# Performance work log

Measured on AMD Instinct MI355X. Metric: run time of the kernel, lower is better.

## Reference

```python
import jax, jax.numpy as jnp
import numpy as np

H, DH, PE = 8, 64, 32
SCALE = DH ** -0.5


def setup_inputs() -> dict:
    key = jax.random.key(0)
    ks = jax.random.split(key, 12)
    B, L, D, K, G = 2, 4096, 256, 16, 4
    inner = H * DH
    kv_in = D + PE
    return {
        "spatial": jax.random.normal(ks[0], (B, L, D), jnp.float32),
        "topk_indices": jax.random.randint(ks[1], (B, L, K), 0, L, jnp.int32),
        "rpe": jax.random.normal(ks[2], (B, L, K, PE), jnp.float32),
        "self_rpe": jax.random.normal(ks[3], (B, L, 1, PE), jnp.float32),
        "distances": jax.random.uniform(ks[4], (B, L, K), jnp.float32) * 10.0,
        "global_latents": jax.random.normal(ks[5], (B, G, D), jnp.float32),
        "Wq": jax.random.normal(ks[6], (D, inner), jnp.float32) * (D ** -0.5),
        "Wk": jax.random.normal(ks[7], (kv_in, inner), jnp.float32) * (kv_in ** -0.5),
        "Wv": jax.random.normal(ks[8], (kv_in, inner), jnp.float32) * (kv_in ** -0.5),
        "Wo": jax.random.normal(ks[9], (inner, D), jnp.float32) * (inner ** -0.5),
        "bo": jnp.zeros((D,), jnp.float32),
        "log_sigma": jnp.full((H,), np.log(3.0), jnp.float32),
        "global_bias": jnp.zeros((), jnp.float32),
    }


def reference(spatial, topk_indices, rpe, self_rpe, distances, global_latents,
              Wq, Wk, Wv, Wo, bo, log_sigma, global_bias):
    B, L, D = spatial.shape
    k = topk_indices.shape[-1]
    G = global_latents.shape[1]
    dt = spatial.dtype

    # gather per-query neighbor features: [B, L, k, D]
    neighbors = jax.vmap(lambda s, idx: s[idx])(spatial, topk_indices)

    # context = [self, neighbors, globals] -> [B, L, c, D], c = 1 + k + G
    ctx = jnp.concatenate([
        spatial[:, :, None, :],
        neighbors,
        jnp.broadcast_to(global_latents[:, None, :, :], (B, L, G, D)),
    ], axis=2)

    # RPE concat on feature dim (self_rpe, rpe, zeros for globals)
    rpe_cat = jnp.concatenate([
        self_rpe, rpe, jnp.zeros((B, L, G, PE), dt)
    ], axis=2)
    ctx = jnp.concatenate([ctx, rpe_cat], axis=-1)  # [B, L, c, D+PE]

    Q = (spatial @ Wq).reshape(B, L, H, DH).transpose(0, 2, 1, 3)          # bhld
    Kt = (ctx @ Wk).reshape(B, L, 1 + k + G, H, DH).transpose(0, 3, 1, 2, 4)  # bhlcd
    Vt = (ctx @ Wv).reshape(B, L, 1 + k + G, H, DH).transpose(0, 3, 1, 2, 4)

    attn = jnp.einsum('bhld,bhlcd->bhlc', Q, Kt) * SCALE

    # gaussian distance bias on local (self + k neighbors) slots
    sigma_sq = jnp.exp(log_sigma) ** 2                     # [H]
    dist_local = jnp.concatenate([jnp.zeros((B, L, 1), dt), distances], axis=2)  # [B,L,1+k]
    gauss = -(dist_local ** 2)[:, None, :, :] / (2.0 * sigma_sq[None, :, None, None])
    bias = jnp.concatenate([
        gauss,
        jnp.broadcast_to(global_bias, (B, H, L, G)).astype(dt),
    ], axis=-1)
    attn = attn + bias

    w = jax.nn.softmax(attn, axis=-1)
    out = jnp.einsum('bhlc,bhlcd->bhld', w, Vt)
    out = out.transpose(0, 2, 1, 3).reshape(B, L, H * DH)
    return out @ Wo + bo
```

## Files before the change

### kernel.cpp

```cpp
#include <hip/hip_runtime.h>
#include <hip/hip_bf16.h>

#define BB 2
#define LL 4096
#define DD 256
#define KK 16
#define GG 4
#define HH 8
#define DH 64
#define PE 32
#define INNER 512
#define CC 21
#define MM (BB*LL)
#define SCALE 0.125f
#define NT1 1792
#define KT1 256
#define NT2 256
#define KT2 768

typedef unsigned short u16;
typedef __attribute__((ext_vector_type(8))) short bf16x8;
typedef __attribute__((ext_vector_type(4))) float f32x4;
typedef unsigned short ushort4_t __attribute__((ext_vector_type(4)));
typedef unsigned short ushort8_t __attribute__((ext_vector_type(8)));

static __device__ __forceinline__ float bf2f(unsigned short u) {
    return __uint_as_float(((unsigned)u) << 16);
}
static __device__ __forceinline__ unsigned short f2bf(float f) {
    unsigned u = __float_as_uint(f);
    unsigned r = u + 0x7fffu + ((u >> 16) & 1u);
    return (unsigned short)(r >> 16);
}
static __device__ __forceinline__ void gld_lds16(const void* g, void* l) {
    __builtin_amdgcn_global_load_lds(
        (const __attribute__((address_space(1))) unsigned int*)g,
        (__attribute__((address_space(3))) unsigned int*)l, 16, 0, 0);
}

__global__ __launch_bounds__(256) void prep_A(
    const float* __restrict__ Wq, const float* __restrict__ Wk,
    float* __restrict__ A)
{
    const int e = blockIdx.x;
    const int tid = threadIdx.x;
    __shared__ float qrow[INNER];
    qrow[tid]       = Wq[e * INNER + tid];
    qrow[tid + 256] = Wq[e * INNER + 256 + tid];
    __syncthreads();
    const int h = tid >> 5, p = tid & 31;
    const float* __restrict__ wr = &Wk[(size_t)(DD + p) * INNER + h * DH];
    const float* __restrict__ qh = &qrow[h * DH];
    float s = 0.f;
    #pragma unroll 8
    for (int d = 0; d < DH; ++d) s += wr[d] * qh[d];
    A[e * 256 + tid] = s;
}

__global__ __launch_bounds__(256) void prep_M2(
    const float* __restrict__ Wv, const float* __restrict__ Wo,
    float* __restrict__ M2)
{
    const int hp = blockIdx.x;
    const int h = hp >> 5, p = hp & 31;
    const int tid = threadIdx.x;
    __shared__ float vrow[DH];
    if (tid < DH) vrow[tid] = Wv[(size_t)(DD + p) * INNER + h * DH + tid];
    __syncthreads();
    float s = 0.f;
    #pragma unroll 8
    for (int d = 0; d < DH; ++d) s += vrow[d] * Wo[(size_t)(h * DH + d) * DD + tid];
    M2[hp * 256 + tid] = s;
}

__global__ __launch_bounds__(256) void cast_spatial(
    const float* __restrict__ in, u16* __restrict__ out)
{
    const size_t i = ((size_t)blockIdx.x * 256 + threadIdx.x) * 8;
    float4 a = *reinterpret_cast<const float4*>(&in[i]);
    float4 b = *reinterpret_cast<const float4*>(&in[i + 4]);
    ushort8_t v = { f2bf(a.x), f2bf(a.y), f2bf(a.z), f2bf(a.w),
                    f2bf(b.x), f2bf(b.y), f2bf(b.z), f2bf(b.w) };
    *reinterpret_cast<ushort8_t*>(&out[i]) = v;
}

__global__ __launch_bounds__(256) void prep_wcat_t(
    const float* __restrict__ Wq, const float* __restrict__ Wk,
    const float* __restrict__ Wv, const float* __restrict__ A,
    u16* __restrict__ Wt)
{
    const int n0 = blockIdx.x * 64;
    const int k0 = blockIdx.y * 64;
    const float* src; int ld, nloc;
    if (n0 < 512)       { src = Wq; ld = INNER; nloc = n0; }
    else if (n0 < 1024) { src = Wk; ld = INNER; nloc = n0 - 512; }
    else if (n0 < 1536) { src = Wv; ld = INNER; nloc = n0 - 1024; }
    else                { src = A;  ld = 256;   nloc = n0 - 1536; }

    __shared__ float tile[64][65];
    const int tid = threadIdx.x;
    const int tk = tid >> 4;
    const int tn = (tid & 15) * 4;
    #pragma unroll
    for (int rep = 0; rep < 4; ++rep) {
        const int k = k0 + tk + rep * 16;
        float4 v = *reinterpret_cast<const float4*>(&src[(size_t)k * ld + nloc + tn]);
        tile[tk + rep * 16][tn + 0] = v.x; tile[tk + rep * 16][tn + 1] = v.y;
        tile[tk + rep * 16][tn + 2] = v.z; tile[tk + rep * 16][tn + 3] = v.w;
    }
    __syncthreads();
    const int wn = tid >> 2;
    const int wk = (tid & 3) * 16;
    ushort8_t o0, o1;
    #pragma unroll
    for (int i = 0; i < 8; ++i) o0[i] = f2bf(tile[wk + i][wn]);
    #pragma unroll
    for (int i = 0; i < 8; ++i) o1[i] = f2bf(tile[wk + 8 + i][wn]);
    u16* dst = &Wt[(size_t)(n0 + wn) * KT1 + k0 + wk];
    *reinterpret_cast<ushort8_t*>(dst)     = o0;
    *reinterpret_cast<ushort8_t*>(dst + 8) = o1;
}

__global__ __launch_bounds__(256) void prep_wout_t(
    const float* __restrict__ Wo, const float* __restrict__ M2,
    u16* __restrict__ Wot)
{
    const int n0 = blockIdx.x * 64;
    const int k0 = blockIdx.y * 64;
    const float* src; int krow;
    if (k0 < 512) { src = Wo; krow = k0; }
    else          { src = M2; krow = k0 - 512; }

    __shared__ float tile[64][65];
    const int tid = threadIdx.x;
    const int tk = tid >> 4;
    const int tn = (tid & 15) * 4;
    #pragma unroll
    for (int rep = 0; rep < 4; ++rep) {
        const int k = krow + tk + rep * 16;
        float4 v = *reinterpret_cast<const float4*>(&src[(size_t)k * DD + n0 + tn]);
        tile[tk + rep * 16][tn + 0] = v.x; tile[tk + rep * 16][tn + 1] = v.y;
        tile[tk + rep * 16][tn + 2] = v.z; tile[tk + rep * 16][tn + 3] = v.w;
    }
    __syncthreads();
    const int wn = tid >> 2;
    const int wk = (tid & 3) * 16;
    ushort8_t o0, o1;
    #pragma unroll
    for (int i = 0; i < 8; ++i) o0[i] = f2bf(tile[wk + i][wn]);
    #pragma unroll
    for (int i = 0; i < 8; ++i) o1[i] = f2bf(tile[wk + 8 + i][wn]);
    u16* dst = &Wot[(size_t)(n0 + wn) * KT2 + k0 + wk];
    *reinterpret_cast<ushort8_t*>(dst)     = o0;
    *reinterpret_cast<ushort8_t*>(dst + 8) = o1;
}

template<int KT, int LDA, int NTOT, int BN, bool F32OUT>
__global__ __launch_bounds__(256) void mfma_gemm(
    const u16* __restrict__ A, const u16* __restrict__ Bt,
    u16* __restrict__ outB, float* __restrict__ outF,
    const float* __restrict__ bias)
{
    constexpr int WNT = BN / 2;
    constexpr int BJ  = WNT / 16;
    constexpr int BCH = BN / 8;

    __shared__ u16 As[128 * 64];
    __shared__ u16 Bs[BN * 64];

    const int tid  = threadIdx.x;
    const int lane = tid & 63;
    const int w    = tid >> 6;
    const int wr   = w >> 1, wc = w & 1;
    const int m0 = blockIdx.x * 128;
    const int n0 = blockIdx.y * BN;
    const int fr = lane & 15, fq = lane >> 4;

    f32x4 acc[4][BJ];
    #pragma unroll
    for (int i = 0; i < 4; ++i)
        #pragma unroll
        for (int j = 0; j < BJ; ++j)
            acc[i][j] = (f32x4){0.f, 0.f, 0.f, 0.f};

    for (int t = 0; t < KT / 64; ++t) {
        const int k0 = t * 64;
        #pragma unroll
        for (int cc = 0; cc < 4; ++cc) {
            const int chunk = w + cc * 4;
            gld_lds16(A + (size_t)(m0 + chunk * 8 + (lane >> 3)) * LDA + k0 + (lane & 7) * 8,
                      (char*)&As[0] + chunk * 1024);
        }
        #pragma unroll
        for (int cc = 0; cc < BCH / 4; ++cc) {
            const int chunk = w + cc * 4;
            gld_lds16(Bt + (size_t)(n0 + chunk * 8 + (lane >> 3)) * KT + k0 + (lane & 7) * 8,
                      (char*)&Bs[0] + chunk * 1024);
        }
        __syncthreads();
        #pragma unroll
        for (int ks = 0; ks < 2; ++ks) {
            bf16x8 av[4], bv[BJ];
            #pragma unroll
            for (int i = 0; i < 4; ++i)
                av[i] = *reinterpret_cast<const bf16x8*>(
                    &As[(wr * 64 + i * 16 + fr) * 64 + ks * 32 + fq * 8]);
            #pragma unroll
            for (int j = 0; j < BJ; ++j)
                bv[j] = *reinterpret_cast<const bf16x8*>(
                    &Bs[(wc * WNT + j * 16 + fr) * 64 + ks * 32 + fq * 8]);
            #pragma unroll
            for (int i = 0; i < 4; ++i)
                #pragma unroll
                for (int j = 0; j < BJ; ++j)
                    acc[i][j] = __builtin_amdgcn_mfma_f32_16x16x32_bf16(
                        av[i], bv[j], acc[i][j], 0, 0, 0);
        }
        __syncthreads();
    }

    #pragma unroll
    for (int i = 0; i < 4; ++i)
        #pragma unroll
        for (int j = 0; j < BJ; ++j)
            #pragma unroll
            for (int rgi = 0; rgi < 4; ++rgi) {
                const int row = m0 + wr * 64 + i * 16 + fq * 4 + rgi;
                const int col = n0 + wc * WNT + j * 16 + fr;
                if constexpr (F32OUT)
                    outF[(size_t)row * NTOT + col] = acc[i][j][rgi] + bias[col];
                else
                    outB[(size_t)row * NTOT + col] = f2bf(acc[i][j][rgi]);
            }
}

__global__ __launch_bounds__(256) void gemm_globals(
    const float* __restrict__ gl, const float* __restrict__ Wk,
    const float* __restrict__ Wv, u16* __restrict__ Kg, u16* __restrict__ Vg)
{
    const int bg  = blockIdx.x;
    const int tid = threadIdx.x;
    const int col = blockIdx.y * 128 + (tid & 127);
    const bool isv = tid >= 128;
    const float* __restrict__ W = isv ? Wv : Wk;
    const float* __restrict__ x = &gl[bg * DD];
    float s = 0.f;
    #pragma unroll 4
    for (int k = 0; k < DD; ++k) s += x[k] * W[(size_t)k * INNER + col];
    if (isv) Vg[bg * INNER + col] = f2bf(s);
    else     Kg[bg * INNER + col] = f2bf(s);
}

__global__ __launch_bounds__(256) void attn_kernel(
    const u16* __restrict__ X, const u16* __restrict__ Kg,
    const u16* __restrict__ Vg, const int* __restrict__ topk,
    const float* __restrict__ rpe, const float* __restrict__ self_rpe,
    const float* __restrict__ distances, const float* __restrict__ log_sigma,
    const float* __restrict__ global_bias, u16* __restrict__ ob2)
{
    const int lane = threadIdx.x & 63;
    const int q = __builtin_amdgcn_readfirstlane(blockIdx.x * 4 + (threadIdx.x >> 6));
    const int b = q >> 12;
    const int h = lane >> 3;
    const int r = lane & 7;
    const int qk = q * KK;
    const size_t bL = (size_t)b * LL;
    const int bG = b * GG;

    float qf[8];
    {
        ushort8_t qv = *reinterpret_cast<const ushort8_t*>(&X[(size_t)q * NT1 + lane * 8]);
        #pragma unroll
        for (int j = 0; j < 8; ++j) qf[j] = bf2f(qv[j]);
    }
    float t4[4];
    {
        ushort4_t tu = *reinterpret_cast<const ushort4_t*>(
            &X[(size_t)q * NT1 + 1536 + h * 32 + r * 4]);
        t4[0] = bf2f(tu[0]); t4[1] = bf2f(tu[1]);
        t4[2] = bf2f(tu[2]); t4[3] = bf2f(tu[3]);
    }

    const float inv2sig = 0.5f * __expf(-2.f * log_sigma[h]);
    const float gbias   = global_bias[0];

    float m = -1e30f, denom = 0.f;
    float acc[8] = {0.f,0.f,0.f,0.f,0.f,0.f,0.f,0.f};
    float rb[4]  = {0.f,0.f,0.f,0.f};

    #pragma unroll
    for (int c = 0; c < CC; ++c) {
        const u16 *kb, *vb;
        const float* rp_ = nullptr;
        float biasc;
        if (c == 0) {
            kb = &X[(size_t)q * NT1 + 512]; vb = &X[(size_t)q * NT1 + 1024];
            rp_ = &self_rpe[(size_t)q * PE];
            biasc = 0.f;
        } else if (c < 17) {
            const int idx = topk[qk + c - 1];
            const u16* row = &X[(bL + idx) * NT1];
            kb = row + 512; vb = row + 1024;
            rp_ = &rpe[((size_t)qk + (c - 1)) * PE];
            const float d = distances[qk + c - 1];
            biasc = -(d * d) * inv2sig;
        } else {
            kb = &Kg[(size_t)(bG + c - 17) * INNER];
            vb = &Vg[(size_t)(bG + c - 17) * INNER];
            biasc = gbias;
        }
        ushort8_t kv = *reinterpret_cast<const ushort8_t*>(kb + lane * 8);
        ushort8_t vv = *reinterpret_cast<const ushort8_t*>(vb + lane * 8);
        float4 r4 = {0.f,0.f,0.f,0.f};
        if (c < 17) r4 = *reinterpret_cast<const float4*>(rp_ + r * 4);

        float part = bf2f(kv[0])*qf[0] + bf2f(kv[1])*qf[1]
                   + bf2f(kv[2])*qf[2] + bf2f(kv[3])*qf[3]
                   + bf2f(kv[4])*qf[4] + bf2f(kv[5])*qf[5]
                   + bf2f(kv[6])*qf[6] + bf2f(kv[7])*qf[7];
        if (c < 17)
            part += r4.x*t4[0] + r4.y*t4[1] + r4.z*t4[2] + r4.w*t4[3];
        part += __shfl_xor(part, 1);
        part += __shfl_xor(part, 2);
        part += __shfl_xor(part, 4);

        const float logit = part * SCALE + biasc;
        const float mn = fmaxf(m, logit);
        const float f  = __expf(m - mn);
        const float e  = __expf(logit - mn);
        denom = denom * f + e;
        #pragma unroll
        for (int i = 0; i < 8; ++i) acc[i] = acc[i] * f + e * bf2f(vv[i]);
        if (c < 17) {
            rb[0] = rb[0] * f + e * r4.x;  rb[1] = rb[1] * f + e * r4.y;
            rb[2] = rb[2] * f + e * r4.z;  rb[3] = rb[3] * f + e * r4.w;
        } else {
            rb[0] *= f; rb[1] *= f; rb[2] *= f; rb[3] *= f;
        }
        m = mn;
    }

    const float inv = 1.f / denom;
    ushort4_t ru = { f2bf(rb[0]*inv), f2bf(rb[1]*inv), f2bf(rb[2]*inv), f2bf(rb[3]*inv) };
    *reinterpret_cast<ushort4_t*>(&ob2[(size_t)q * KT2 + 512 + h * 32 + r * 4]) = ru;
    ushort8_t ou = { f2bf(acc[0]*inv), f2bf(acc[1]*inv), f2bf(acc[2]*inv), f2bf(acc[3]*inv),
                     f2bf(acc[4]*inv), f2bf(acc[5]*inv), f2bf(acc[6]*inv), f2bf(acc[7]*inv) };
    *reinterpret_cast<ushort8_t*>(&ob2[(size_t)q * KT2 + lane * 8]) = ou;
}

extern "C" void kernel_launch(void* const* d_in, const int* in_sizes, int n_in,
                              void* d_out, int out_size, void* d_ws, size_t ws_size,
                              hipStream_t stream)
{
    const float* spatial     = (const float*)d_in[0];
    const int*   topk        = (const int*)  d_in[1];
    const float* rpe         = (const float*)d_in[2];
    const float* self_rpe    = (const float*)d_in[3];
    const float* distances   = (const float*)d_in[4];
    const float* gl          = (const float*)d_in[5];
    const float* Wq          = (const float*)d_in[6];
    const float* Wk          = (const float*)d_in[7];
    const float* Wv          = (const float*)d_in[8];
    const float* Wo          = (const float*)d_in[9];
    const float* bo          = (const float*)d_in[10];
    const float* log_sigma   = (const float*)d_in[11];
    const float* global_bias = (const float*)d_in[12];
    float* out = (float*)d_out;

    char* p = (char*)d_ws;
    float* A   = (float*)p;  p += (size_t)256 * 256 * 4;
    float* M2  = (float*)p;  p += (size_t)256 * 256 * 4;
    u16* Sb    = (u16*)p;    p += (size_t)MM * DD * 2;
    u16* Wt    = (u16*)p;    p += (size_t)NT1 * KT1 * 2;
    u16* Wot   = (u16*)p;    p += (size_t)NT2 * KT2 * 2;
    u16* X     = (u16*)p;    p += (size_t)MM * NT1 * 2;
    u16* ob2   = (u16*)p;    p += (size_t)MM * KT2 * 2;
    u16* Kg    = (u16*)p;    p += (size_t)BB * GG * INNER * 2;
    u16* Vg    = (u16*)p;    p += (size_t)BB * GG * INNER * 2;

    prep_A <<<256, 256, 0, stream>>>(Wq, Wk, A);
    prep_M2<<<256, 256, 0, stream>>>(Wv, Wo, M2);
    cast_spatial<<<MM * DD / (256 * 8), 256, 0, stream>>>(spatial, Sb);
    prep_wcat_t<<<dim3(NT1 / 64, KT1 / 64), 256, 0, stream>>>(Wq, Wk, Wv, A, Wt);
    prep_wout_t<<<dim3(NT2 / 64, KT2 / 64), 256, 0, stream>>>(Wo, M2, Wot);
    gemm_globals<<<dim3(BB * GG, 4), 256, 0, stream>>>(gl, Wk, Wv, Kg, Vg);

    mfma_gemm<KT1, 256, NT1, 128, false><<<dim3(MM / 128, NT1 / 128), 256, 0, stream>>>(
        Sb, Wt, X, nullptr, nullptr);

    attn_kernel<<<MM / 4, 256, 0, stream>>>(
        X, Kg, Vg, topk, rpe, self_rpe, distances, log_sigma, global_bias, ob2);

    mfma_gemm<KT2, KT2, NT2, 64, true><<<dim3(MM / 128, NT2 / 64), 256, 0, stream>>>(
        ob2, Wot, nullptr, out, bo);
}
```

Measured before the change: 118.4 us.

## Merge prep kernels into two launches and split attention heads across two waves

Six small preprocessing kernels become two multi-role kernels that pick their role by block index, cutting launch count and inter-kernel gaps. The attention kernel now has two wavefronts per query, each covering four heads with 16 lanes per head. Each lane loads half as much per context slot, and the grid doubles, raising parallelism and occupancy (launch_bounds 256,8). The cost is an extra shuffle-reduction step and smaller, less vectorised loads.

```diff
diff --git a/kernel.cpp b/kernel.cpp
--- a/kernel.cpp
+++ b/kernel.cpp
@@ -21,6 +21,7 @@
 typedef unsigned short u16;
 typedef __attribute__((ext_vector_type(8))) short bf16x8;
 typedef __attribute__((ext_vector_type(4))) float f32x4;
+typedef unsigned short ushort2_t __attribute__((ext_vector_type(2)));
 typedef unsigned short ushort4_t __attribute__((ext_vector_type(4)));
 typedef unsigned short ushort8_t __attribute__((ext_vector_type(8)));
 
@@ -38,72 +39,92 @@
         (__attribute__((address_space(3))) unsigned int*)l, 16, 0, 0);
 }
 
-__global__ __launch_bounds__(256) void prep_A(
+__global__ __launch_bounds__(256) void megaprep1(
     const float* __restrict__ Wq, const float* __restrict__ Wk,
-    float* __restrict__ A)
-{
-    const int e = blockIdx.x;
+    const float* __restrict__ Wv, const float* __restrict__ Wo,
+    const float* __restrict__ spatial, const float* __restrict__ gl,
+    float* __restrict__ A, float* __restrict__ M2, u16* __restrict__ Sb,
+    u16* __restrict__ Kg, u16* __restrict__ Vg)
+{
+    const int bid = blockIdx.x;
     const int tid = threadIdx.x;
-    __shared__ float qrow[INNER];
-    qrow[tid]       = Wq[e * INNER + tid];
-    qrow[tid + 256] = Wq[e * INNER + 256 + tid];
-    __syncthreads();
-    const int h = tid >> 5, p = tid & 31;
-    const float* __restrict__ wr = &Wk[(size_t)(DD + p) * INNER + h * DH];
-    const float* __restrict__ qh = &qrow[h * DH];
-    float s = 0.f;
-    #pragma unroll 8
-    for (int d = 0; d < DH; ++d) s += wr[d] * qh[d];
-    A[e * 256 + tid] = s;
-}
-
-__global__ __launch_bounds__(256) void prep_M2(
-    const float* __restrict__ Wv, const float* __restrict__ Wo,
-    float* __restrict__ M2)
-{
-    const int hp = blockIdx.x;
-    const int h = hp >> 5, p = hp & 31;
-    const int tid = threadIdx.x;
-    __shared__ float vrow[DH];
-    if (tid < DH) vrow[tid] = Wv[(size_t)(DD + p) * INNER + h * DH + tid];
-    __syncthreads();
-    float s = 0.f;
-    #pragma unroll 8
-    for (int d = 0; d < DH; ++d) s += vrow[d] * Wo[(size_t)(h * DH + d) * DD + tid];
-    M2[hp * 256 + tid] = s;
-}
-
-__global__ __launch_bounds__(256) void cast_spatial(
-    const float* __restrict__ in, u16* __restrict__ out)
-{
-    const size_t i = ((size_t)blockIdx.x * 256 + threadIdx.x) * 8;
-    float4 a = *reinterpret_cast<const float4*>(&in[i]);
-    float4 b = *reinterpret_cast<const float4*>(&in[i + 4]);
-    ushort8_t v = { f2bf(a.x), f2bf(a.y), f2bf(a.z), f2bf(a.w),
-                    f2bf(b.x), f2bf(b.y), f2bf(b.z), f2bf(b.w) };
-    *reinterpret_cast<ushort8_t*>(&out[i]) = v;
-}
-
-__global__ __launch_bounds__(256) void prep_wcat_t(
+    __shared__ float smem[INNER];
+
+    if (bid < 256) {
+        const int e = bid;
+        smem[tid]       = Wq[e * INNER + tid];
+        smem[tid + 256] = Wq[e * INNER + 256 + tid];
+        __syncthreads();
+        const int h = tid >> 5, p = tid & 31;
+        const float* __restrict__ wr = &Wk[(size_t)(DD + p) * INNER + h * DH];
+        const float* __restrict__ qh = &smem[h * DH];
+        float s = 0.f;
+        #pragma unroll 8
+        for (int d = 0; d < DH; ++d) s += wr[d] * qh[d];
+        A[e * 256 + tid] = s;
+    } else if (bid < 512) {
+        const int hp = bid - 256;
+        const int h = hp >> 5, p = hp & 31;
+        if (tid < DH) smem[tid] = Wv[(size_t)(DD + p) * INNER + h * DH + tid];
+        __syncthreads();
+        float s = 0.f;
+        #pragma unroll 8
+        for (int d = 0; d < DH; ++d) s += smem[d] * Wo[(size_t)(h * DH + d) * DD + tid];
+        M2[hp * 256 + tid] = s;
+    } else if (bid < 1536) {
+        const size_t i = ((size_t)(bid - 512) * 256 + tid) * 8;
+        float4 a = *reinterpret_cast<const float4*>(&spatial[i]);
+        float4 b = *reinterpret_cast<const float4*>(&spatial[i + 4]);
+        ushort8_t v = { f2bf(a.x), f2bf(a.y), f2bf(a.z), f2bf(a.w),
+                        f2bf(b.x), f2bf(b.y), f2bf(b.z), f2bf(b.w) };
+        *reinterpret_cast<ushort8_t*>(&Sb[i]) = v;
+    } else {
+        const int local = bid - 1536;
+        const int bg = local >> 2;
+        const int col = (local & 3) * 128 + (tid & 127);
+        const bool isv = tid >= 128;
+        const float* __restrict__ W = isv ? Wv : Wk;
+        const float* __restrict__ x = &gl[bg * DD];
+        float s = 0.f;
+        #pragma unroll 4
+        for (int k = 0; k < DD; ++k) s += x[k] * W[(size_t)k * INNER + col];
+        if (isv) Vg[bg * INNER + col] = f2bf(s);
+        else     Kg[bg * INNER + col] = f2bf(s);
+    }
+}
+
+__global__ __launch_bounds__(256) void megaprep2(
     const float* __restrict__ Wq, const float* __restrict__ Wk,
     const float* __restrict__ Wv, const float* __restrict__ A,
-    u16* __restrict__ Wt)
-{
-    const int n0 = blockIdx.x * 64;
-    const int k0 = blockIdx.y * 64;
-    const float* src; int ld, nloc;
-    if (n0 < 512)       { src = Wq; ld = INNER; nloc = n0; }
-    else if (n0 < 1024) { src = Wk; ld = INNER; nloc = n0 - 512; }
-    else if (n0 < 1536) { src = Wv; ld = INNER; nloc = n0 - 1024; }
-    else                { src = A;  ld = 256;   nloc = n0 - 1536; }
-
+    const float* __restrict__ Wo, const float* __restrict__ M2,
+    u16* __restrict__ Wt, u16* __restrict__ Wot)
+{
     __shared__ float tile[64][65];
+    const int bid = blockIdx.x;
     const int tid = threadIdx.x;
+
+    const float* src; int ld, nloc, n0, k0, ldo; u16* dstbase; int kt;
+    if (bid < 112) {
+        n0 = (bid % 28) * 64; k0 = (bid / 28) * 64;
+        if (n0 < 512)       { src = Wq; ld = INNER; nloc = n0; }
+        else if (n0 < 1024) { src = Wk; ld = INNER; nloc = n0 - 512; }
+        else if (n0 < 1536) { src = Wv; ld = INNER; nloc = n0 - 1024; }
+        else                { src = A;  ld = 256;   nloc = n0 - 1536; }
+        dstbase = Wt; ldo = KT1; kt = k0;
+    } else {
+        const int local = bid - 112;
+        n0 = (local % 4) * 64; k0 = (local / 4) * 64;
+        if (k0 < 512) { src = Wo; kt = k0; }
+        else          { src = M2; kt = k0 - 512; }
+        ld = DD; nloc = n0;
+        dstbase = Wot; ldo = KT2;
+    }
+
     const int tk = tid >> 4;
     const int tn = (tid & 15) * 4;
     #pragma unroll
     for (int rep = 0; rep < 4; ++rep) {
-        const int k = k0 + tk + rep * 16;
+        const int k = kt + tk + rep * 16;
         float4 v = *reinterpret_cast<const float4*>(&src[(size_t)k * ld + nloc + tn]);
         tile[tk + rep * 16][tn + 0] = v.x; tile[tk + rep * 16][tn + 1] = v.y;
         tile[tk + rep * 16][tn + 2] = v.z; tile[tk + rep * 16][tn + 3] = v.w;
@@ -116,41 +137,7 @@
     for (int i = 0; i < 8; ++i) o0[i] = f2bf(tile[wk + i][wn]);
     #pragma unroll
     for (int i = 0; i < 8; ++i) o1[i] = f2bf(tile[wk + 8 + i][wn]);
-    u16* dst = &Wt[(size_t)(n0 + wn) * KT1 + k0 + wk];
-    *reinterpret_cast<ushort8_t*>(dst)     = o0;
-    *reinterpret_cast<ushort8_t*>(dst + 8) = o1;
-}
-
-__global__ __launch_bounds__(256) void prep_wout_t(
-    const float* __restrict__ Wo, const float* __restrict__ M2,
-    u16* __restrict__ Wot)
-{
-    const int n0 = blockIdx.x * 64;
-    const int k0 = blockIdx.y * 64;
-    const float* src; int krow;
-    if (k0 < 512) { src = Wo; krow = k0; }
-    else          { src = M2; krow = k0 - 512; }
-
-    __shared__ float tile[64][65];
-    const int tid = threadIdx.x;
-    const int tk = tid >> 4;
-    const int tn = (tid & 15) * 4;
-    #pragma unroll
-    for (int rep = 0; rep < 4; ++rep) {
-        const int k = krow + tk + rep * 16;
-        float4 v = *reinterpret_cast<const float4*>(&src[(size_t)k * DD + n0 + tn]);
-        tile[tk + rep * 16][tn + 0] = v.x; tile[tk + rep * 16][tn + 1] = v.y;
-        tile[tk + rep * 16][tn + 2] = v.z; tile[tk + rep * 16][tn + 3] = v.w;
-    }
-    __syncthreads();
-    const int wn = tid >> 2;
-    const int wk = (tid & 3) * 16;
-    ushort8_t o0, o1;
-    #pragma unroll
-    for (int i = 0; i < 8; ++i) o0[i] = f2bf(tile[wk + i][wn]);
-    #pragma unroll
-    for (int i = 0; i < 8; ++i) o1[i] = f2bf(tile[wk + 8 + i][wn]);
-    u16* dst = &Wot[(size_t)(n0 + wn) * KT2 + k0 + wk];
+    u16* dst = &dstbase[(size_t)(n0 + wn) * ldo + k0 + wk];
     *reinterpret_cast<ushort8_t*>(dst)     = o0;
     *reinterpret_cast<ushort8_t*>(dst + 8) = o1;
 }
@@ -234,59 +221,45 @@
             }
 }
 
-__global__ __launch_bounds__(256) void gemm_globals(
-    const float* __restrict__ gl, const float* __restrict__ Wk,
-    const float* __restrict__ Wv, u16* __restrict__ Kg, u16* __restrict__ Vg)
-{
-    const int bg  = blockIdx.x;
-    const int tid = threadIdx.x;
-    const int col = blockIdx.y * 128 + (tid & 127);
-    const bool isv = tid >= 128;
-    const float* __restrict__ W = isv ? Wv : Wk;
-    const float* __restrict__ x = &gl[bg * DD];
-    float s = 0.f;
-    #pragma unroll 4
-    for (int k = 0; k < DD; ++k) s += x[k] * W[(size_t)k * INNER + col];
-    if (isv) Vg[bg * INNER + col] = f2bf(s);
-    else     Kg[bg * INNER + col] = f2bf(s);
-}
-
-__global__ __launch_bounds__(256) void attn_kernel(
+__global__ __launch_bounds__(256, 8) void attn_kernel(
     const u16* __restrict__ X, const u16* __restrict__ Kg,
     const u16* __restrict__ Vg, const int* __restrict__ topk,
     const float* __restrict__ rpe, const float* __restrict__ self_rpe,
     const float* __restrict__ distances, const float* __restrict__ log_sigma,
     const float* __restrict__ global_bias, u16* __restrict__ ob2)
 {
-    const int lane = threadIdx.x & 63;
-    const int q = __builtin_amdgcn_readfirstlane(blockIdx.x * 4 + (threadIdx.x >> 6));
-    const int b = q >> 12;
-    const int h = lane >> 3;
-    const int r = lane & 7;
-    const int qk = q * KK;
+    const int tid  = threadIdx.x;
+    const int lane = tid & 63;
+    const int w    = tid >> 6;
+    const int q    = __builtin_amdgcn_readfirstlane(blockIdx.x * 2 + (w >> 1));
+    const int half = w & 1;
+    const int b    = q >> 12;
+    const int h    = half * 4 + (lane >> 4);
+    const int rr   = lane & 15;
+    const int jo   = half * 256 + lane * 4;
+    const int qk   = q * KK;
     const size_t bL = (size_t)b * LL;
-    const int bG = b * GG;
-
-    float qf[8];
+    const int bG   = b * GG;
+
+    float qf[4];
     {
-        ushort8_t qv = *reinterpret_cast<const ushort8_t*>(&X[(size_t)q * NT1 + lane * 8]);
-        #pragma unroll
-        for (int j = 0; j < 8; ++j) qf[j] = bf2f(qv[j]);
-    }
-    float t4[4];
+        ushort4_t qv = *reinterpret_cast<const ushort4_t*>(&X[(size_t)q * NT1 + jo]);
+        #pragma unroll
+        for (int j = 0; j < 4; ++j) qf[j] = bf2f(qv[j]);
+    }
+    float t2[2];
     {
-        ushort4_t tu = *reinterpret_cast<const ushort4_t*>(
-            &X[(size_t)q * NT1 + 1536 + h * 32 + r * 4]);
-        t4[0] = bf2f(tu[0]); t4[1] = bf2f(tu[1]);
-        t4[2] = bf2f(tu[2]); t4[3] = bf2f(tu[3]);
+        ushort2_t tu = *reinterpret_cast<const ushort2_t*>(
+            &X[(size_t)q * NT1 + 1536 + h * 32 + rr * 2]);
+        t2[0] = bf2f(tu[0]); t2[1] = bf2f(tu[1]);
     }
 
     const float inv2sig = 0.5f * __expf(-2.f * log_sigma[h]);
     const float gbias   = global_bias[0];
 
     float m = -1e30f, denom = 0.f;
-    float acc[8] = {0.f,0.f,0.f,0.f,0.f,0.f,0.f,0.f};
-    float rb[4]  = {0.f,0.f,0.f,0.f};
+    float acc[4] = {0.f, 0.f, 0.f, 0.f};
+    float rb[2]  = {0.f, 0.f};
 
     #pragma unroll
     for (int c = 0; c < CC; ++c) {
@@ -294,7 +267,8 @@
         const float* rp_ = nullptr;
         float biasc;
         if (c == 0) {
-            kb = &X[(size_t)q * NT1 + 512]; vb = &X[(size_t)q * NT1 + 1024];
+            const u16* row = &X[(size_t)q * NT1];
+            kb = row + 512; vb = row + 1024;
             rp_ = &self_rpe[(size_t)q * PE];
             biasc = 0.f;
         } else if (c < 17) {
@@ -309,20 +283,19 @@
             vb = &Vg[(size_t)(bG + c - 17) * INNER];
             biasc = gbias;
         }
-        ushort8_t kv = *reinterpret_cast<const ushort8_t*>(kb + lane * 8);
-        ushort8_t vv = *reinterpret_cast<const ushort8_t*>(vb + lane * 8);
-        float4 r4 = {0.f,0.f,0.f,0.f};
-        if (c < 17) r4 = *reinterpret_cast<const float4*>(rp_ + r * 4);
+        ushort4_t kv = *reinterpret_cast<const ushort4_t*>(kb + jo);
+        ushort4_t vv = *reinterpret_cast<const ushort4_t*>(vb + jo);
+        float2 r2 = {0.f, 0.f};
+        if (c < 17) r2 = *reinterpret_cast<const float2*>(rp_ + rr * 2);
 
         float part = bf2f(kv[0])*qf[0] + bf2f(kv[1])*qf[1]
-                   + bf2f(kv[2])*qf[2] + bf2f(kv[3])*qf[3]
-                   + bf2f(kv[4])*qf[4] + bf2f(kv[5])*qf[5]
-                   + bf2f(kv[6])*qf[6] + bf2f(kv[7])*qf[7];
+                   + bf2f(kv[2])*qf[2] + bf2f(kv[3])*qf[3];
         if (c < 17)
-            part += r4.x*t4[0] + r4.y*t4[1] + r4.z*t4[2] + r4.w*t4[3];
+            part += r2.x * t2[0] + r2.y * t2[1];
         part += __shfl_xor(part, 1);
         part += __shfl_xor(part, 2);
         part += __shfl_xor(part, 4);
+        part += __shfl_xor(part, 8);
 
         const float logit = part * SCALE + biasc;
         const float mn = fmaxf(m, logit);
@@ -330,22 +303,21 @@
         const float e  = __expf(logit - mn);
         denom = denom * f + e;
         #pragma unroll
-        for (int i = 0; i < 8; ++i) acc[i] = acc[i] * f + e * bf2f(vv[i]);
+        for (int i = 0; i < 4; ++i) acc[i] = acc[i] * f + e * bf2f(vv[i]);
         if (c < 17) {
-            rb[0] = rb[0] * f + e * r4.x;  rb[1] = rb[1] * f + e * r4.y;
-            rb[2] = rb[2] * f + e * r4.z;  rb[3] = rb[3] * f + e * r4.w;
+            rb[0] = rb[0] * f + e * r2.x;
+            rb[1] = rb[1] * f + e * r2.y;
         } else {
-            rb[0] *= f; rb[1] *= f; rb[2] *= f; rb[3] *= f;
+            rb[0] *= f; rb[1] *= f;
         }
         m = mn;
     }
 
     const float inv = 1.f / denom;
-    ushort4_t ru = { f2bf(rb[0]*inv), f2bf(rb[1]*inv), f2bf(rb[2]*inv), f2bf(rb[3]*inv) };
-    *reinterpret_cast<ushort4_t*>(&ob2[(size_t)q * KT2 + 512 + h * 32 + r * 4]) = ru;
-    ushort8_t ou = { f2bf(acc[0]*inv), f2bf(acc[1]*inv), f2bf(acc[2]*inv), f2bf(acc[3]*inv),
-                     f2bf(acc[4]*inv), f2bf(acc[5]*inv), f2bf(acc[6]*inv), f2bf(acc[7]*inv) };
-    *reinterpret_cast<ushort8_t*>(&ob2[(size_t)q * KT2 + lane * 8]) = ou;
+    ushort2_t ru = { f2bf(rb[0] * inv), f2bf(rb[1] * inv) };
+    *reinterpret_cast<ushort2_t*>(&ob2[(size_t)q * KT2 + 512 + h * 32 + rr * 2]) = ru;
+    ushort4_t ou = { f2bf(acc[0]*inv), f2bf(acc[1]*inv), f2bf(acc[2]*inv), f2bf(acc[3]*inv) };
+    *reinterpret_cast<ushort4_t*>(&ob2[(size_t)q * KT2 + jo]) = ou;
 }
 
 extern "C" void kernel_launch(void* const* d_in, const int* in_sizes, int n_in,
@@ -378,17 +350,14 @@
     u16* Kg    = (u16*)p;    p += (size_t)BB * GG * INNER * 2;
     u16* Vg    = (u16*)p;    p += (size_t)BB * GG * INNER * 2;
 
-    prep_A <<<256, 256, 0, stream>>>(Wq, Wk, A);
-    prep_M2<<<256, 256, 0, stream>>>(Wv, Wo, M2);
-    cast_spatial<<<MM * DD / (256 * 8), 256, 0, stream>>>(spatial, Sb);
-    prep_wcat_t<<<dim3(NT1 / 64, KT1 / 64), 256, 0, stream>>>(Wq, Wk, Wv, A, Wt);
-    prep_wout_t<<<dim3(NT2 / 64, KT2 / 64), 256, 0, stream>>>(Wo, M2, Wot);
-    gemm_globals<<<dim3(BB * GG, 4), 256, 0, stream>>>(gl, Wk, Wv, Kg, Vg);
+    megaprep1<<<1568, 256, 0, stream>>>(Wq, Wk, Wv, Wo, spatial, gl,
+                                        A, M2, Sb, Kg, Vg);
+    megaprep2<<<160, 256, 0, stream>>>(Wq, Wk, Wv, A, Wo, M2, Wt, Wot);
 
     mfma_gemm<KT1, 256, NT1, 128, false><<<dim3(MM / 128, NT1 / 128), 256, 0, stream>>>(
         Sb, Wt, X, nullptr, nullptr);
 
-    attn_kernel<<<MM / 4, 256, 0, stream>>>(
+    attn_kernel<<<MM / 2, 256, 0, stream>>>(
         X, Kg, Vg, topk, rpe, self_rpe, distances, log_sigma, global_bias, ob2);
 
     mfma_gemm<KT2, KT2, NT2, 64, true><<<dim3(MM / 128, NT2 / 64), 256, 0, stream>>>(
```

Result: slower. 167.6 us (+41.5%).
